# Performance work log

Measured on AMD Instinct MI355X. Metric: run time of the kernel, lower is better.

## Reference

```python
import jax, jax.numpy as jnp
import numpy as np

D_MODEL = 768
D_HIDDEN = 2048
N_HEADS = 12
D_HEAD = 64
REG_COEFF = 1e-3
EPS = 1e-6
BATCH = 4
SEQ = 128


def setup_inputs() -> dict:
    key = jax.random.key(0)
    ks = jax.random.split(key, 4)
    # kaiming_uniform_ on (fan_in, fan_out)-shaped tensors: bound = sqrt(6 / fan_in_torch)
    # (values only need to be plausible; exact init dist is irrelevant for the kernel baseline)
    s_enc = 1.0 / np.sqrt(D_MODEL)
    s_dec = 1.0 / np.sqrt(D_HIDDEN)
    return {
        "x": jax.random.normal(ks[0], (BATCH, SEQ, D_MODEL), dtype=jnp.float32),
        "W_encQ": jax.random.normal(ks[1], (D_MODEL, D_HIDDEN), dtype=jnp.float32) * s_enc,
        "W_encK": jax.random.normal(ks[2], (D_MODEL, D_HIDDEN), dtype=jnp.float32) * s_enc,
        "b_encQ": jnp.zeros((D_HIDDEN,), dtype=jnp.float32),
        "b_encK": jnp.zeros((D_HIDDEN,), dtype=jnp.float32),
        "W_dec": jax.random.normal(ks[3], (D_HIDDEN, N_HEADS), dtype=jnp.float32) * s_dec,
        "b_dec": jnp.zeros((N_HEADS,), dtype=jnp.float32),
    }


def reference(x, W_encQ, W_encK, b_encQ, b_encK, W_dec, b_dec):
    # queries/keys: (batch, posn, d_hidden)
    queries = jax.nn.relu(jnp.einsum("bsd,dh->bsh", x, W_encQ) + b_encQ)
    keys = jax.nn.relu(jnp.einsum("bsd,dh->bsh", x, W_encK) + b_encK)
    # acts: (batch, posn_q, posn_k, d_hidden) -- the huge multi-use intermediate
    acts = queries[:, :, None, :] * keys[:, None, :, :]
    reg_loss = REG_COEFF * jnp.sum(jnp.sqrt(jnp.abs(acts) + EPS))
    feature_fires = (acts > 0).astype(jnp.int32)
    # decode to per-head scores: (batch, posn_q, posn_k, n_heads)
    score = jnp.einsum("bqkh,hn->bqkn", acts, W_dec) / np.sqrt(D_HEAD) + b_dec
    score = jnp.transpose(score, (0, 3, 1, 2))  # (batch, n_heads, posn_q, posn_k)
    return score, reg_loss, feature_fires
```

## Files before the change

kernel.cpp:

```cpp
#include <hip/hip_runtime.h>
#include <hip/hip_bf16.h>

#define D_MODEL 768
#define D_HIDDEN 2048
#define NHEADS 12
#define BATCH 4
#define SEQ 128
#define MROWS (BATCH*SEQ)
#define SCORE_ELEMS (BATCH*NHEADS*SEQ*SEQ)
#define REG_OFF SCORE_ELEMS
#define FIRES_OFF (SCORE_ELEMS + 1)
#define NROWS_T 65536
#define FIRES_WAVES 2048
#define FIRES_BLOCKS 512
#define SCORE_BLOCKS (BATCH*NHEADS*16)
#define TRIGCAP 64

typedef __attribute__((ext_vector_type(8))) short bf16x8;
typedef __attribute__((ext_vector_type(4))) float f32x4;

static __device__ __forceinline__ unsigned short f2bf(float f) {
    union { float f; unsigned u; } v; v.f = f;
    unsigned u = v.u;
    return (unsigned short)((u + 0x7FFFu + ((u >> 16) & 1u)) >> 16);
}

static __device__ __forceinline__ void split_bf16(float v, short& hi, short& lo) {
    unsigned short h = f2bf(v);
    float hf = __uint_as_float((unsigned)h << 16);
    float lf = v - hf;
    hi = (short)h;
    lo = (short)f2bf(lf);
}

static __device__ __forceinline__ float fsqrt_fast(float x) {
    return __builtin_amdgcn_sqrtf(x);
}

__global__ __launch_bounds__(256) void enc_kernel(
    const float* __restrict__ x,
    const float* __restrict__ WQ, const float* __restrict__ WK,
    const float* __restrict__ bQ, const float* __restrict__ bK,
    float* __restrict__ qbuf, float* __restrict__ kbuf)
{
    __shared__ unsigned tcnt;
    __shared__ unsigned tlist[TRIGCAP];
    __shared__ double   redd[4];

    const int bufid = blockIdx.z;
    const float* W    = bufid ? WK : WQ;
    const float* bias = bufid ? bK : bQ;
    float* outbuf     = bufid ? kbuf : qbuf;

    const int t  = threadIdx.x;
    if (t == 0) tcnt = 0u;
    __syncthreads();

    const int w  = t >> 6;
    const int l  = t & 63;
    const int mt = blockIdx.y * 64 + (w >> 1) * 32;
    const int nt = blockIdx.x * 64 + (w & 1) * 32;
    const int lr = l & 15;
    const int hg = (l >> 4) * 8;

    f32x4 acc[2][2];
    #pragma unroll
    for (int i = 0; i < 2; ++i)
        #pragma unroll
        for (int j = 0; j < 2; ++j) { f32x4 z = {0.f, 0.f, 0.f, 0.f}; acc[i][j] = z; }

    for (int kk = 0; kk < D_MODEL; kk += 32) {
        const int h0 = kk + hg;
        bf16x8 ah[2], al[2], bh[2], bl[2];
        #pragma unroll
        for (int fi = 0; fi < 2; ++fi) {
            const float* xp = x + (size_t)(mt + fi * 16 + lr) * D_MODEL + h0;
            const float4 v1 = *reinterpret_cast<const float4*>(xp);
            const float4 v2 = *reinterpret_cast<const float4*>(xp + 4);
            const float vv[8] = {v1.x, v1.y, v1.z, v1.w, v2.x, v2.y, v2.z, v2.w};
            #pragma unroll
            for (int i = 0; i < 8; ++i) {
                short h_, lo_;
                split_bf16(vv[i], h_, lo_);
                ah[fi][i] = h_; al[fi][i] = lo_;
            }
        }
        #pragma unroll
        for (int fj = 0; fj < 2; ++fj) {
            const int col = nt + fj * 16 + lr;
            #pragma unroll
            for (int i = 0; i < 8; ++i) {
                short h_, lo_;
                split_bf16(W[(size_t)(h0 + i) * D_HIDDEN + col], h_, lo_);
                bh[fj][i] = h_; bl[fj][i] = lo_;
            }
        }
        #pragma unroll
        for (int fi = 0; fi < 2; ++fi)
            #pragma unroll
            for (int fj = 0; fj < 2; ++fj) {
                acc[fi][fj] = __builtin_amdgcn_mfma_f32_16x16x32_bf16(
                    ah[fi], bh[fj], acc[fi][fj], 0, 0, 0);
                acc[fi][fj] = __builtin_amdgcn_mfma_f32_16x16x32_bf16(
                    ah[fi], bl[fj], acc[fi][fj], 0, 0, 0);
                acc[fi][fj] = __builtin_amdgcn_mfma_f32_16x16x32_bf16(
                    al[fi], bh[fj], acc[fi][fj], 0, 0, 0);
            }
    }

    #pragma unroll
    for (int fi = 0; fi < 2; ++fi)
        #pragma unroll
        for (int fj = 0; fj < 2; ++fj)
            #pragma unroll
            for (int j = 0; j < 4; ++j) {
                const int row = mt + fi * 16 + (l >> 4) * 4 + j;
                const int col = nt + fj * 16 + lr;
                float pre = acc[fi][fj][j] + bias[col];
                if (fabsf(pre) < 3e-4f) {
                    unsigned idx = atomicAdd(&tcnt, 1u);
                    if (idx < TRIGCAP) {
                        tlist[idx] = ((unsigned)row << 11) | (unsigned)col;
                    } else {
                        const float* xr = x + (size_t)row * D_MODEL;
                        const float* wc = W + col;
                        double s = (double)bias[col];
                        for (int dd = 0; dd < D_MODEL; ++dd)
                            s += (double)xr[dd] * (double)wc[(size_t)dd * D_HIDDEN];
                        pre = (float)s;
                    }
                }
                outbuf[(size_t)row * D_HIDDEN + col] = fmaxf(pre, 0.f);
            }

    __syncthreads();
    const unsigned n = min(tcnt, (unsigned)TRIGCAP);
    for (unsigned i = 0; i < n; ++i) {
        const unsigned e = tlist[i];
        const int hh = (int)(e & 2047u);
        const int mm = (int)(e >> 11);
        double s = 0.0;
        #pragma unroll
        for (int k = 0; k < 3; ++k) {
            const int dd = t + k * 256;
            s += (double)x[(size_t)mm * D_MODEL + dd]
               * (double)W[(size_t)dd * D_HIDDEN + hh];
        }
        #pragma unroll
        for (int off = 32; off > 0; off >>= 1) s += __shfl_down(s, off);
        if (l == 0) redd[w] = s;
        __syncthreads();
        if (t == 0) {
            double tot = redd[0] + redd[1] + redd[2] + redd[3] + (double)bias[hh];
            outbuf[(size_t)mm * D_HIDDEN + hh] = fmaxf((float)tot, 0.f);
        }
        __syncthreads();
    }
}

__global__ __launch_bounds__(256) void prep_kernel(
    const float* __restrict__ qbuf, const float* __restrict__ kbuf,
    unsigned* __restrict__ qmask, unsigned* __restrict__ kmask,
    float* __restrict__ sq, float* __restrict__ sk,
    float* __restrict__ nzq, float* __restrict__ nzk)
{
    const int bi = blockIdx.x;
    const int t  = threadIdx.x;

    if (bi < MROWS) {
        if (t >= 128) return;
        const int r = bi;
        const int l = t & 63;
        const float* src = (t < 64) ? qbuf : kbuf;
        unsigned* dst    = (t < 64) ? qmask : kmask;
        unsigned m = 0;
        #pragma unroll
        for (int j = 0; j < 8; ++j)
            #pragma unroll
            for (int e = 0; e < 4; ++e) {
                const float v = src[(size_t)r * D_HIDDEN + 256 * j + 4 * l + e];
                m |= (v > 0.f ? 1u : 0u) << (4 * j + e);
            }
        dst[r * 64 + l] = m;
        return;
    }

    const int cid = bi - MROWS;
    const int buf = cid >> 6;
    const int idx = cid & 63;
    const int b   = idx >> 4;
    const int rg  = idx & 15;
    const float* src = buf ? kbuf : qbuf;
    float* S  = buf ? sk  : sq;
    float* NZ = buf ? nzk : nzq;

    const int h0 = t * 8;
    float s[8]  = {0, 0, 0, 0, 0, 0, 0, 0};
    float nz[8] = {0, 0, 0, 0, 0, 0, 0, 0};
    #pragma unroll
    for (int rr = 0; rr < 8; ++rr) {
        const int row = b * SEQ + rg * 8 + rr;
        const float* p = src + (size_t)row * D_HIDDEN + h0;
        const f32x4 v1 = *reinterpret_cast<const f32x4*>(p);
        const f32x4 v2 = *reinterpret_cast<const f32x4*>(p + 4);
        #pragma unroll
        for (int e = 0; e < 4; ++e) {
            s[e]      += fsqrt_fast(v1[e]);
            nz[e]     += (v1[e] > 0.f) ? 1.f : 0.f;
            s[e + 4]  += fsqrt_fast(v2[e]);
            nz[e + 4] += (v2[e] > 0.f) ? 1.f : 0.f;
        }
    }
    #pragma unroll
    for (int e = 0; e < 8; ++e) {
        atomicAdd(&S[b * D_HIDDEN + h0 + e], s[e]);
        atomicAdd(&NZ[b * D_HIDDEN + h0 + e], nz[e]);
    }
}

__global__ __launch_bounds__(256) void main_kernel(
    const float* __restrict__ qbuf, const float* __restrict__ kbuf,
    const unsigned* __restrict__ qmask, const unsigned* __restrict__ kmask,
    const float* __restrict__ sq, const float* __restrict__ sk,
    const float* __restrict__ nzq, const float* __restrict__ nzk,
    const float* __restrict__ Wdec, const float* __restrict__ bdec,
    float* __restrict__ out)
{
    __shared__ float wcol[D_HIDDEN];
    __shared__ float red[4][64][16];
    const int t  = threadIdx.x;
    const int bi = blockIdx.x;
    const int w  = t >> 6;
    const int l  = t & 63;

    if (bi < FIRES_BLOCKS) {
        const int g  = bi * 4 + w;
        const int g7 = g >> 7;
        const int gk = g & 127;

        f32x4* out4 = reinterpret_cast<f32x4*>(out + FIRES_OFF - 1);

        #pragma unroll 1
        for (int b = 0; b < 4; ++b) {
            const unsigned km = kmask[(b * SEQ + gk) * 64 + l];

            #pragma unroll 1
            for (int ss = 0; ss < 8; ++ss) {
                const int s    = b * 8 + ss;
                const int R    = g + s * FIRES_WAVES;
                const int brow = s * 16 + g7;
                const unsigned qm = qmask[brow * 64 + l];
                const unsigned m   = qm & km;
                const unsigned mp  = __shfl_up(m, 1);
                const unsigned m63 = __shfl(m, 63);

                unsigned pb1 = 0;
                if (l == 0 && R > 0) {
                    const int pbrow = (R - 1) >> 7;
                    const int pb    = pbrow >> 7;
                    const int pkrow = (pb << 7) + ((R - 1) & 127);
                    pb1 = (qmask[pbrow * 64 + 63] >> 31)
                        & (kmask[pkrow * 64 + 63] >> 31) & 1u;
                }

                #pragma unroll
                for (int j = 0; j < 8; ++j) {
                    unsigned b0;
                    if (l == 0) b0 = (j == 0) ? pb1 : (m63 >> (4 * (j - 1) + 3)) & 1u;
                    else        b0 = (mp >> (4 * j + 3)) & 1u;
                    f32x4 f;
                    f[0] = b0 ? 1.f : 0.f;
                    f[1] = ((m >> (4 * j + 0)) & 1u) ? 1.f : 0.f;
                    f[2] = ((m >> (4 * j + 1)) & 1u) ? 1.f : 0.f;
                    f[3] = ((m >> (4 * j + 2)) & 1u) ? 1.f : 0.f;
                    if (R == 0 && j == 0 && l == 0) {
                        out[FIRES_OFF + 0] = f[1];
                        out[FIRES_OFF + 1] = f[2];
                        out[FIRES_OFF + 2] = f[3];
                    } else {
                        __builtin_nontemporal_store(f, &out4[(size_t)R * 512 + 64 * j + l]);
                    }
                }
            }
        }

        if (bi == FIRES_BLOCKS - 1 && w == 3 && l == 0) {
            const float pv = qbuf[(size_t)511 * D_HIDDEN + 2047]
                           * kbuf[(size_t)511 * D_HIDDEN + 2047];
            out[(size_t)(FIRES_OFF - 1) + (size_t)NROWS_T * D_HIDDEN] = (pv > 0.f) ? 1.f : 0.f;
        }
        return;
    }

    if (bi < FIRES_BLOCKS + SCORE_BLOCKS) {
        const int sb  = bi - FIRES_BLOCKS;
        const int sub = sb & 15;
        const int pr  = sb >> 4;
        const int n   = pr % NHEADS;
        const int b   = pr / NHEADS;

        for (int idx = t; idx < D_HIDDEN; idx += 256)
            wcol[idx] = Wdec[(size_t)idx * NHEADS + n];
        __syncthreads();

        const int qt   = (sub >> 2) * 32;
        const int kt   = (sub & 3) * 32;
        const int lrow = l & 15;
        const int koff = (l >> 4) * 8;

        f32x4 acc[2][2];
        #pragma unroll
        for (int i = 0; i < 2; ++i)
            #pragma unroll
            for (int j = 0; j < 2; ++j) { f32x4 z = {0.f, 0.f, 0.f, 0.f}; acc[i][j] = z; }

        const float* qb = qbuf + (size_t)b * SEQ * D_HIDDEN;
        const float* kb = kbuf + (size_t)b * SEQ * D_HIDDEN;

        const int hlo = w * 512;
        for (int kk = hlo; kk < hlo + 512; kk += 32) {
            const int h0 = kk + koff;
            float wv[8];
            #pragma unroll
            for (int i = 0; i < 8; ++i) wv[i] = wcol[h0 + i];

            bf16x8 afrag[2], bfrag[2];
            #pragma unroll
            for (int fi = 0; fi < 2; ++fi) {
                const float* qp = qb + (size_t)(qt + fi * 16 + lrow) * D_HIDDEN + h0;
                const float4 q1 = *reinterpret_cast<const float4*>(qp);
                const float4 q2 = *reinterpret_cast<const float4*>(qp + 4);
                const float qf[8] = {q1.x, q1.y, q1.z, q1.w, q2.x, q2.y, q2.z, q2.w};
                #pragma unroll
                for (int i = 0; i < 8; ++i) afrag[fi][i] = (short)f2bf(qf[i] * wv[i]);
            }
            #pragma unroll
            for (int fj = 0; fj < 2; ++fj) {
                const float* kp = kb + (size_t)(kt + fj * 16 + lrow) * D_HIDDEN + h0;
                const float4 k1 = *reinterpret_cast<const float4*>(kp);
                const float4 k2 = *reinterpret_cast<const float4*>(kp + 4);
                const float kf[8] = {k1.x, k1.y, k1.z, k1.w, k2.x, k2.y, k2.z, k2.w};
                #pragma unroll
                for (int i = 0; i < 8; ++i) bfrag[fj][i] = (short)f2bf(kf[i]);
            }
            #pragma unroll
            for (int fi = 0; fi < 2; ++fi)
                #pragma unroll
                for (int fj = 0; fj < 2; ++fj)
                    acc[fi][fj] = __builtin_amdgcn_mfma_f32_16x16x32_bf16(
                        afrag[fi], bfrag[fj], acc[fi][fj], 0, 0, 0);
        }

        #pragma unroll
        for (int fi = 0; fi < 2; ++fi)
            #pragma unroll
            for (int fj = 0; fj < 2; ++fj)
                #pragma unroll
                for (int j = 0; j < 4; ++j)
                    red[w][l][fi * 8 + fj * 4 + j] = acc[fi][fj][j];
        __syncthreads();

        const float bd   = bdec[n];
        const int   outb = (b * NHEADS + n) * SEQ * SEQ;
        #pragma unroll
        for (int u = 0; u < 4; ++u) {
            const int j = w * 4 + u;
            const float s = (red[0][l][j] + red[1][l][j])
                          + (red[2][l][j] + red[3][l][j]);
            const int fi = j >> 3, fj = (j >> 2) & 1, jj = j & 3;
            const int row = qt + fi * 16 + (l >> 4) * 4 + jj;
            const int col = kt + fj * 16 + (l & 15);
            out[outb + row * SEQ + col] = s * 0.125f + bd;
        }
        return;
    }

    {
        __shared__ double rd[4];
        double acc = 0.0;
        for (int i = t; i < BATCH * D_HIDDEN; i += 256) {
            const float zc = 16384.f - nzq[i] * nzk[i];
            acc += (double)(sq[i] * sk[i] + zc * 1e-3f);
        }
        #pragma unroll
        for (int off = 32; off > 0; off >>= 1) acc += __shfl_down(acc, off);
        if (l == 0) rd[w] = acc;
        __syncthreads();
        if (t == 0)
            out[REG_OFF] = (float)((rd[0] + rd[1] + rd[2] + rd[3]) * 1e-3);
    }
}

extern "C" void kernel_launch(void* const* d_in, const int* in_sizes, int n_in,
                              void* d_out, int out_size, void* d_ws, size_t ws_size,
                              hipStream_t stream) {
    const float* x  = (const float*)d_in[0];
    const float* WQ = (const float*)d_in[1];
    const float* WK = (const float*)d_in[2];
    const float* bQ = (const float*)d_in[3];
    const float* bK = (const float*)d_in[4];
    const float* Wd = (const float*)d_in[5];
    const float* bd = (const float*)d_in[6];
    float* out  = (float*)d_out;
    float* qbuf = (float*)d_ws;
    float* kbuf = qbuf + (size_t)MROWS * D_HIDDEN;
    unsigned* qmask = (unsigned*)(kbuf + (size_t)MROWS * D_HIDDEN);
    unsigned* kmask = qmask + (size_t)MROWS * 64;
    float* sq  = (float*)(kmask + (size_t)MROWS * 64);
    float* sk  = sq  + BATCH * D_HIDDEN;
    float* nzq = sk  + BATCH * D_HIDDEN;
    float* nzk = nzq + BATCH * D_HIDDEN;

    dim3 b256(256);

    (void)hipMemsetAsync(sq, 0, (size_t)4 * BATCH * D_HIDDEN * sizeof(float), stream);

    enc_kernel<<<dim3(D_HIDDEN / 64, MROWS / 64, 2), b256, 0, stream>>>(
        x, WQ, WK, bQ, bK, qbuf, kbuf);

    prep_kernel<<<dim3(MROWS + 128), b256, 0, stream>>>(
        qbuf, kbuf, qmask, kmask, sq, sk, nzq, nzk);

    main_kernel<<<dim3(FIRES_BLOCKS + SCORE_BLOCKS + 1), b256, 0, stream>>>(
        qbuf, kbuf, qmask, kmask, sq, sk, nzq, nzk, Wd, bd, out);
}
```

Before: 171.3 us.

## Pre-split inputs and weights to bf16 hi/lo with transposed layout before encoder GEMM

Adds a prep kernel that splits x and the encoder weights into bf16 high/low parts once per call, storing the weights transposed so both GEMM operands are K-contiguous. A new encoder kernel then loads these precomputed bf16 tiles and runs three-term split-bf16 MFMAs, so the float-to-bf16 splitting no longer happens inside the GEMM inner loop. Near-zero pre-activations are still recomputed in double precision. The trade-off is an extra launch and extra workspace traffic for the split copies, and the new path only runs when the workspace is large enough.

```diff
diff --git a/kernel.cpp b/kernel.cpp
--- a/kernel.cpp
+++ b/kernel.cpp
@@ -17,6 +17,7 @@
 #define TRIGCAP 64
 
 typedef __attribute__((ext_vector_type(8))) short bf16x8;
+typedef __attribute__((ext_vector_type(4))) short bf16x4;
 typedef __attribute__((ext_vector_type(4))) float f32x4;
 
 static __device__ __forceinline__ unsigned short f2bf(float f) {
@@ -35,6 +36,202 @@
 
 static __device__ __forceinline__ float fsqrt_fast(float x) {
     return __builtin_amdgcn_sqrtf(x);
+}
+
+__global__ __launch_bounds__(256) void prep_split_kernel(
+    const float* __restrict__ x,
+    const float* __restrict__ WQ, const float* __restrict__ WK,
+    unsigned short* __restrict__ xh, unsigned short* __restrict__ xl,
+    unsigned short* __restrict__ WQhT, unsigned short* __restrict__ WQlT,
+    unsigned short* __restrict__ WKhT, unsigned short* __restrict__ WKlT)
+{
+    const int bi = blockIdx.x;
+    const int t  = threadIdx.x;
+
+    if (bi < 768) {
+        __shared__ float tile[64][68];
+        const int wz  = bi / 384;
+        const int rem = bi % 384;
+        const int h0  = (rem % 12) * 64;
+        const int n0  = (rem / 12) * 64;
+        const float* W = wz ? WK : WQ;
+        unsigned short* dh = wz ? WKhT : WQhT;
+        unsigned short* dl = wz ? WKlT : WQlT;
+
+        #pragma unroll
+        for (int u = 0; u < 4; ++u) {
+            const int fid = t + 256 * u;
+            const int h   = fid >> 4;
+            const int c4  = (fid & 15) * 4;
+            *reinterpret_cast<f32x4*>(&tile[h][c4]) =
+                *reinterpret_cast<const f32x4*>(&W[(size_t)(h0 + h) * D_HIDDEN + n0 + c4]);
+        }
+        __syncthreads();
+        #pragma unroll
+        for (int u = 0; u < 4; ++u) {
+            const int fid = t + 256 * u;
+            const int n   = fid >> 4;
+            const int h4  = (fid & 15) * 4;
+            bf16x4 vh, vl;
+            #pragma unroll
+            for (int e = 0; e < 4; ++e) {
+                short hh, ll;
+                split_bf16(tile[h4 + e][n], hh, ll);
+                vh[e] = hh; vl[e] = ll;
+            }
+            const size_t o = (size_t)(n0 + n) * D_MODEL + h0 + h4;
+            *reinterpret_cast<bf16x4*>(&dh[o]) = vh;
+            *reinterpret_cast<bf16x4*>(&dl[o]) = vl;
+        }
+        return;
+    }
+
+    for (int fid = (bi - 768) * 256 + t; fid < (MROWS * D_MODEL) / 4; fid += 32 * 256) {
+        const f32x4 v = *reinterpret_cast<const f32x4*>(&x[(size_t)fid * 4]);
+        bf16x4 vh, vl;
+        #pragma unroll
+        for (int e = 0; e < 4; ++e) {
+            short hh, ll;
+            split_bf16(v[e], hh, ll);
+            vh[e] = hh; vl[e] = ll;
+        }
+        *reinterpret_cast<bf16x4*>(&xh[(size_t)fid * 4]) = vh;
+        *reinterpret_cast<bf16x4*>(&xl[(size_t)fid * 4]) = vl;
+    }
+}
+
+__global__ __launch_bounds__(256) void enc_fast_kernel(
+    const unsigned short* __restrict__ xh, const unsigned short* __restrict__ xl,
+    const unsigned short* __restrict__ WQhT, const unsigned short* __restrict__ WQlT,
+    const unsigned short* __restrict__ WKhT, const unsigned short* __restrict__ WKlT,
+    const float* __restrict__ x,
+    const float* __restrict__ WQ, const float* __restrict__ WK,
+    const float* __restrict__ bQ, const float* __restrict__ bK,
+    float* __restrict__ qbuf, float* __restrict__ kbuf)
+{
+    __shared__ short xsh[64][40], xsl[64][40];
+    __shared__ short wsh[64][40], wsl[64][40];
+    __shared__ unsigned tcnt;
+    __shared__ unsigned tlist[TRIGCAP];
+    __shared__ double   redd[4];
+
+    const int bufid = blockIdx.z;
+    const unsigned short* Wh = bufid ? WKhT : WQhT;
+    const unsigned short* Wl = bufid ? WKlT : WQlT;
+    const float* Wf   = bufid ? WK : WQ;
+    const float* bias = bufid ? bK : bQ;
+    float* outbuf     = bufid ? kbuf : qbuf;
+
+    const int t  = threadIdx.x;
+    if (t == 0) tcnt = 0u;
+
+    const int w  = t >> 6;
+    const int l  = t & 63;
+    const int m0 = blockIdx.y * 64;
+    const int n0 = blockIdx.x * 64;
+    const int mt = (w >> 1) * 32;
+    const int nt = (w & 1) * 32;
+    const int lr = l & 15;
+    const int hg = (l >> 4) * 8;
+
+    f32x4 acc[2][2];
+    #pragma unroll
+    for (int i = 0; i < 2; ++i)
+        #pragma unroll
+        for (int j = 0; j < 2; ++j) { f32x4 z = {0.f, 0.f, 0.f, 0.f}; acc[i][j] = z; }
+
+    for (int kk = 0; kk < D_MODEL; kk += 32) {
+        __syncthreads();
+        #pragma unroll
+        for (int u = 0; u < 2; ++u) {
+            const int fid = t + 256 * u;
+            const int row = fid >> 3;
+            const int c4  = (fid & 7) * 4;
+            const size_t xo = (size_t)(m0 + row) * D_MODEL + kk + c4;
+            *reinterpret_cast<bf16x4*>(&xsh[row][c4]) =
+                *reinterpret_cast<const bf16x4*>(&xh[xo]);
+            *reinterpret_cast<bf16x4*>(&xsl[row][c4]) =
+                *reinterpret_cast<const bf16x4*>(&xl[xo]);
+            const size_t wo = (size_t)(n0 + row) * D_MODEL + kk + c4;
+            *reinterpret_cast<bf16x4*>(&wsh[row][c4]) =
+                *reinterpret_cast<const bf16x4*>(&Wh[wo]);
+            *reinterpret_cast<bf16x4*>(&wsl[row][c4]) =
+                *reinterpret_cast<const bf16x4*>(&Wl[wo]);
+        }
+        __syncthreads();
+
+        bf16x8 ah[2], al[2], bh[2], bl[2];
+        #pragma unroll
+        for (int fi = 0; fi < 2; ++fi) {
+            ah[fi] = *reinterpret_cast<const bf16x8*>(&xsh[mt + fi * 16 + lr][hg]);
+            al[fi] = *reinterpret_cast<const bf16x8*>(&xsl[mt + fi * 16 + lr][hg]);
+        }
+        #pragma unroll
+        for (int fj = 0; fj < 2; ++fj) {
+            bh[fj] = *reinterpret_cast<const bf16x8*>(&wsh[nt + fj * 16 + lr][hg]);
+            bl[fj] = *reinterpret_cast<const bf16x8*>(&wsl[nt + fj * 16 + lr][hg]);
+        }
+        #pragma unroll
+        for (int fi = 0; fi < 2; ++fi)
+            #pragma unroll
+            for (int fj = 0; fj < 2; ++fj) {
+                acc[fi][fj] = __builtin_amdgcn_mfma_f32_16x16x32_bf16(
+                    ah[fi], bh[fj], acc[fi][fj], 0, 0, 0);
+                acc[fi][fj] = __builtin_amdgcn_mfma_f32_16x16x32_bf16(
+                    ah[fi], bl[fj], acc[fi][fj], 0, 0, 0);
+                acc[fi][fj] = __builtin_amdgcn_mfma_f32_16x16x32_bf16(
+                    al[fi], bh[fj], acc[fi][fj], 0, 0, 0);
+            }
+    }
+
+    #pragma unroll
+    for (int fi = 0; fi < 2; ++fi)
+        #pragma unroll
+        for (int fj = 0; fj < 2; ++fj)
+            #pragma unroll
+            for (int j = 0; j < 4; ++j) {
+                const int row = m0 + mt + fi * 16 + (l >> 4) * 4 + j;
+                const int col = n0 + nt + fj * 16 + lr;
+                float pre = acc[fi][fj][j] + bias[col];
+                if (fabsf(pre) < 3e-4f) {
+                    unsigned idx = atomicAdd(&tcnt, 1u);
+                    if (idx < TRIGCAP) {
+                        tlist[idx] = ((unsigned)row << 11) | (unsigned)col;
+                    } else {
+                        const float* xr = x + (size_t)row * D_MODEL;
+                        const float* wc = Wf + col;
+                        double s = (double)bias[col];
+                        for (int dd = 0; dd < D_MODEL; ++dd)
+                            s += (double)xr[dd] * (double)wc[(size_t)dd * D_HIDDEN];
+                        pre = (float)s;
+                    }
+                }
+                outbuf[(size_t)row * D_HIDDEN + col] = fmaxf(pre, 0.f);
+            }
+
+    __syncthreads();
+    const unsigned n = min(tcnt, (unsigned)TRIGCAP);
+    for (unsigned i = 0; i < n; ++i) {
+        const unsigned e = tlist[i];
+        const int hh = (int)(e & 2047u);
+        const int mm = (int)(e >> 11);
+        double s = 0.0;
+        #pragma unroll
+        for (int k = 0; k < 3; ++k) {
+            const int dd = t + k * 256;
+            s += (double)x[(size_t)mm * D_MODEL + dd]
+               * (double)Wf[(size_t)dd * D_HIDDEN + hh];
+        }
+        #pragma unroll
+        for (int off = 32; off > 0; off >>= 1) s += __shfl_down(s, off);
+        if (l == 0) redd[w] = s;
+        __syncthreads();
+        if (t == 0) {
+            double tot = redd[0] + redd[1] + redd[2] + redd[3] + (double)bias[hh];
+            outbuf[(size_t)mm * D_HIDDEN + hh] = fmaxf((float)tot, 0.f);
+        }
+        __syncthreads();
+    }
 }
 
 __global__ __launch_bounds__(256) void enc_kernel(
@@ -402,21 +599,38 @@
     const float* Wd = (const float*)d_in[5];
     const float* bd = (const float*)d_in[6];
     float* out  = (float*)d_out;
-    float* qbuf = (float*)d_ws;
-    float* kbuf = qbuf + (size_t)MROWS * D_HIDDEN;
-    unsigned* qmask = (unsigned*)(kbuf + (size_t)MROWS * D_HIDDEN);
-    unsigned* kmask = qmask + (size_t)MROWS * 64;
-    float* sq  = (float*)(kmask + (size_t)MROWS * 64);
-    float* sk  = sq  + BATCH * D_HIDDEN;
-    float* nzq = sk  + BATCH * D_HIDDEN;
-    float* nzk = nzq + BATCH * D_HIDDEN;
+
+    char* p = (char*)d_ws;
+    float* qbuf = (float*)p;             p += (size_t)MROWS * D_HIDDEN * 4;
+    float* kbuf = (float*)p;             p += (size_t)MROWS * D_HIDDEN * 4;
+    unsigned* qmask = (unsigned*)p;      p += (size_t)MROWS * 64 * 4;
+    unsigned* kmask = (unsigned*)p;      p += (size_t)MROWS * 64 * 4;
+    float* sq  = (float*)p;              p += BATCH * D_HIDDEN * 4;
+    float* sk  = (float*)p;              p += BATCH * D_HIDDEN * 4;
+    float* nzq = (float*)p;              p += BATCH * D_HIDDEN * 4;
+    float* nzk = (float*)p;              p += BATCH * D_HIDDEN * 4;
+    unsigned short* xh   = (unsigned short*)p; p += (size_t)MROWS * D_MODEL * 2;
+    unsigned short* xl   = (unsigned short*)p; p += (size_t)MROWS * D_MODEL * 2;
+    unsigned short* WQhT = (unsigned short*)p; p += (size_t)D_HIDDEN * D_MODEL * 2;
+    unsigned short* WQlT = (unsigned short*)p; p += (size_t)D_HIDDEN * D_MODEL * 2;
+    unsigned short* WKhT = (unsigned short*)p; p += (size_t)D_HIDDEN * D_MODEL * 2;
+    unsigned short* WKlT = (unsigned short*)p; p += (size_t)D_HIDDEN * D_MODEL * 2;
+    const size_t need_full = (size_t)(p - (char*)d_ws);
+    const bool fast = (ws_size >= need_full);
 
     dim3 b256(256);
 
     (void)hipMemsetAsync(sq, 0, (size_t)4 * BATCH * D_HIDDEN * sizeof(float), stream);
 
-    enc_kernel<<<dim3(D_HIDDEN / 64, MROWS / 64, 2), b256, 0, stream>>>(
-        x, WQ, WK, bQ, bK, qbuf, kbuf);
+    if (fast) {
+        prep_split_kernel<<<dim3(800), b256, 0, stream>>>(
+            x, WQ, WK, xh, xl, WQhT, WQlT, WKhT, WKlT);
+        enc_fast_kernel<<<dim3(D_HIDDEN / 64, MROWS / 64, 2), b256, 0, stream>>>(
+            xh, xl, WQhT, WQlT, WKhT, WKlT, x, WQ, WK, bQ, bK, qbuf, kbuf);
+    } else {
+        enc_kernel<<<dim3(D_HIDDEN / 64, MROWS / 64, 2), b256, 0, stream>>>(
+            x, WQ, WK, bQ, bK, qbuf, kbuf);
+    }
 
     prep_kernel<<<dim3(MROWS + 128), b256, 0, stream>>>(
         qbuf, kbuf, qmask, kmask, sq, sk, nzq, nzk);
```

New measurement: 170.0 us. Within noise of the previous version (-0.8%).
